# Performance work log

Measured on AMD Instinct MI355X. Metric: run time of the kernel, lower is better.

## Reference

```python
import jax, jax.numpy as jnp
import numpy as np

N_NODES = 100000
N_EDGES = 1600000
IN_FEAT = 512
HIDDEN = 128
N_CLASSES = 7


def gcn_conv(x, edge_index, edge_weight, W, b):
    """PyG GCNConv: add self-loops (weight 1), symmetric normalization, linear, scatter-add, bias."""
    n = x.shape[0]
    src = jnp.concatenate([edge_index[0], jnp.arange(n, dtype=edge_index.dtype)])
    dst = jnp.concatenate([edge_index[1], jnp.arange(n, dtype=edge_index.dtype)])
    w = jnp.concatenate([edge_weight, jnp.ones((n,), dtype=edge_weight.dtype)])
    deg = jax.ops.segment_sum(w, dst, num_segments=n)  # degree on destination (col)
    dinv = jnp.where(deg > 0, jax.lax.rsqrt(deg), 0.0)
    norm = dinv[src] * w * dinv[dst]                   # [E+N]
    h = x @ W                                          # [N, out] transform BEFORE propagate
    msg = h[src] * norm[:, None]                       # [E+N, out] irregular gather
    out = jax.ops.segment_sum(msg, dst, num_segments=n)  # scatter-reduce
    return out + b


def setup_inputs() -> dict:
    key = jax.random.key(0)
    k1, k2, k3, k4, k5, k6 = jax.random.split(key, 6)
    x = jax.random.normal(k1, (N_NODES, IN_FEAT), dtype=jnp.float32)
    edge_index = jax.random.randint(k2, (2, N_EDGES), 0, N_NODES, dtype=jnp.int32)
    edge_weight = jax.random.uniform(k3, (N_EDGES,), dtype=jnp.float32)
    s1 = 1.0 / np.sqrt(IN_FEAT)
    s2 = 1.0 / np.sqrt(HIDDEN)
    W1 = jax.random.uniform(k4, (IN_FEAT, HIDDEN), dtype=jnp.float32, minval=-s1, maxval=s1)
    b1 = jnp.zeros((HIDDEN,), dtype=jnp.float32)
    W2 = jax.random.uniform(k5, (HIDDEN, N_CLASSES), dtype=jnp.float32, minval=-s2, maxval=s2)
    b2 = jnp.zeros((N_CLASSES,), dtype=jnp.float32)
    return {"x": x, "edge_index": edge_index, "edge_weight": edge_weight,
            "W1": W1, "b1": b1, "W2": W2, "b2": b2}


def reference(x, edge_index, edge_weight, W1, b1, W2, b2):
    # eval mode: F.dropout(training=False) is identity
    h = jax.nn.elu(gcn_conv(x, edge_index, edge_weight, W1, b1))
    out = gcn_conv(h, edge_index, edge_weight, W2, b2)
    return jax.nn.log_softmax(out, axis=1)
```

## Files before the change

kernel.cpp:

```cpp
#include <hip/hip_runtime.h>
#include <hip/hip_bf16.h>
#include <math.h>

#define N_NODES 100000
#define N_EDGES 1600000
#define IN_F 512
#define HID 128
#define NCLS 7

#define DEG_SHIFT 43
#define DEG_WMASK ((1ull << 43) - 1)
#define DEG_SCALE 4194304.0f
#define DEG_INV_SCALE (1.0f / 4194304.0f)

typedef short short8 __attribute__((ext_vector_type(8)));
typedef float f32x4 __attribute__((ext_vector_type(4)));

__device__ __forceinline__ unsigned pack_bf16x2(float a, float b) {
  unsigned ua = __float_as_uint(a), ub = __float_as_uint(b);
  unsigned ra = (ua + 0x7FFFu + ((ua >> 16) & 1u)) >> 16;
  unsigned rb = (ub + 0x7FFFu + ((ub >> 16) & 1u)) >> 16;
  return ra | (rb << 16);
}
__device__ __forceinline__ unsigned short f32_to_bf16(float v) {
  unsigned u = __float_as_uint(v);
  return (unsigned short)((u + 0x7FFFu + ((u >> 16) & 1u)) >> 16);
}
__device__ __forceinline__ float bf_lo(unsigned u) { return __uint_as_float(u << 16); }
__device__ __forceinline__ float bf_hi(unsigned u) { return __uint_as_float(u & 0xFFFF0000u); }

__global__ void k_deg_count(const int* __restrict__ ei, const float* __restrict__ ew,
                            unsigned long long* __restrict__ packed, int* __restrict__ rank) {
  int e = blockIdx.x * blockDim.x + threadIdx.x;
  if (e >= N_EDGES) return;
  int d = ei[N_EDGES + e];
  unsigned long long fx = (unsigned long long)(ew[e] * DEG_SCALE + 0.5f);
  unsigned long long old = atomicAdd(&packed[d], (1ull << DEG_SHIFT) | fx);
  rank[e] = (int)(old >> DEG_SHIFT);
}

__global__ void k_dinv(const unsigned long long* __restrict__ packed,
                       float* __restrict__ dinv, int* __restrict__ cnt,
                       uint2* __restrict__ csr_pad) {
  int i = blockIdx.x * blockDim.x + threadIdx.x;
  if (i < 8) csr_pad[i] = make_uint2(0u, 0u);
  if (i >= N_NODES) return;
  unsigned long long p = packed[i];
  cnt[i] = (int)(p >> DEG_SHIFT);
  float wsum = (float)(p & DEG_WMASK) * DEG_INV_SCALE;
  dinv[i] = rsqrtf(wsum + 1.0f);
}

__global__ void k_w1t(const float* __restrict__ W1, unsigned* __restrict__ w1t_u) {
  int n = blockIdx.x;
  int t = threadIdx.x;
  float a = W1[(size_t)(2 * t) * HID + n];
  float b = W1[(size_t)(2 * t + 1) * HID + n];
  w1t_u[(size_t)n * 256 + t] = pack_bf16x2(a, b);
}

__global__ void k_scan_partial(const int* __restrict__ cnt, int* __restrict__ bsum) {
  __shared__ int s[256];
  int t = threadIdx.x;
  int base = blockIdx.x * 1024;
  int v = 0;
#pragma unroll
  for (int q = 0; q < 4; q++) {
    int idx = base + t * 4 + q;
    if (idx < N_NODES) v += cnt[idx];
  }
  s[t] = v;
  __syncthreads();
  for (int o = 128; o > 0; o >>= 1) {
    if (t < o) s[t] += s[t + o];
    __syncthreads();
  }
  if (t == 0) bsum[blockIdx.x] = s[0];
}

__global__ void k_scan_bsum(int* bsum, int nb) {
  if (threadIdx.x == 0 && blockIdx.x == 0) {
    int acc = 0;
    for (int i = 0; i < nb; i++) { int v = bsum[i]; bsum[i] = acc; acc += v; }
  }
}

__global__ void k_scan_final(const int* __restrict__ cnt, const int* __restrict__ bsum,
                             int* __restrict__ offs) {
  __shared__ int s[256];
  int t = threadIdx.x;
  int base = blockIdx.x * 1024;
  int v[4]; int sum = 0;
#pragma unroll
  for (int q = 0; q < 4; q++) {
    int idx = base + t * 4 + q;
    v[q] = (idx < N_NODES) ? cnt[idx] : 0;
    sum += v[q];
  }
  s[t] = sum;
  __syncthreads();
  for (int o = 1; o < 256; o <<= 1) {
    int x = (t >= o) ? s[t - o] : 0;
    __syncthreads();
    s[t] += x;
    __syncthreads();
  }
  int acc = s[t] - sum + bsum[blockIdx.x];
#pragma unroll
  for (int q = 0; q < 4; q++) {
    int idx = base + t * 4 + q;
    if (idx < N_NODES) offs[idx] = acc;
    acc += v[q];
  }
}

__global__ void k_fill(const int* __restrict__ ei, const float* __restrict__ ew,
                       const int* __restrict__ rank, const int* __restrict__ offs,
                       uint2* __restrict__ csr) {
  int e = blockIdx.x * blockDim.x + threadIdx.x;
  if (e >= N_EDGES) return;
  int sidx = ei[e];
  int d = ei[N_EDGES + e];
  int p = offs[d] + rank[e];
  csr[p] = make_uint2((unsigned)sidx, __float_as_uint(ew[e]));
}

#define G1_LDSROW 20
__global__ __launch_bounds__(256) void k_gemm1(const float* __restrict__ x,
                                               const unsigned* __restrict__ w1t_u,
                                               const float* __restrict__ dinv,
                                               unsigned short* __restrict__ h_u16) {
  __shared__ unsigned As[128 * G1_LDSROW];
  __shared__ unsigned Bs[128 * G1_LDSROW];
  const int tid = threadIdx.x;
  const int lane = tid & 63;
  const int w = tid >> 6;
  const int wr = w >> 1, wc = w & 1;
  const int quad = lane >> 4;
  const int l16 = lane & 15;
  const int m0 = blockIdx.x * 128;

  f32x4 acc[4][4];
#pragma unroll
  for (int i = 0; i < 4; i++)
#pragma unroll
    for (int j = 0; j < 4; j++) acc[i][j] = (f32x4){0.f, 0.f, 0.f, 0.f};

  for (int k0 = 0; k0 < IN_F; k0 += 32) {
    __syncthreads();
#pragma unroll
    for (int q = 0; q < 4; q++) {
      int flat = q * 256 + tid;
      int row = flat >> 3;
      int c4 = flat & 7;
      int gr = m0 + row;
      float4 v = make_float4(0.f, 0.f, 0.f, 0.f);
      if (gr < N_NODES) v = *(const float4*)(x + (size_t)gr * IN_F + k0 + c4 * 4);
      unsigned lo = pack_bf16x2(v.x, v.y);
      unsigned hi = pack_bf16x2(v.z, v.w);
      *(uint2*)&As[row * G1_LDSROW + c4 * 2] = make_uint2(lo, hi);
    }
#pragma unroll
    for (int q = 0; q < 2; q++) {
      int flat = q * 256 + tid;
      int row = flat >> 2;
      int c = flat & 3;
      uint4 bv = ((const uint4*)w1t_u)[(size_t)row * 64 + (k0 >> 3) + c];
      *(uint4*)&Bs[row * G1_LDSROW + c * 4] = bv;
    }
    __syncthreads();
    short8 af[4], bf[4];
#pragma unroll
    for (int mi = 0; mi < 4; mi++)
      af[mi] = *(const short8*)&As[(wr * 64 + mi * 16 + l16) * G1_LDSROW + quad * 4];
#pragma unroll
    for (int ni = 0; ni < 4; ni++)
      bf[ni] = *(const short8*)&Bs[(wc * 64 + ni * 16 + l16) * G1_LDSROW + quad * 4];
#pragma unroll
    for (int mi = 0; mi < 4; mi++)
#pragma unroll
      for (int ni = 0; ni < 4; ni++)
        acc[mi][ni] = __builtin_amdgcn_mfma_f32_16x16x32_bf16(af[mi], bf[ni], acc[mi][ni], 0, 0, 0);
  }
#pragma unroll
  for (int mi = 0; mi < 4; mi++) {
    float df[4];
#pragma unroll
    for (int r = 0; r < 4; r++) {
      int grow = m0 + wr * 64 + mi * 16 + quad * 4 + r;
      df[r] = (grow < N_NODES) ? dinv[grow] : 0.f;
    }
#pragma unroll
    for (int ni = 0; ni < 4; ni++) {
      int gcol = wc * 64 + ni * 16 + l16;
#pragma unroll
      for (int r = 0; r < 4; r++) {
        int grow = m0 + wr * 64 + mi * 16 + quad * 4 + r;
        if (grow < N_NODES)
          h_u16[(size_t)grow * HID + gcol] = f32_to_bf16(acc[mi][ni][r] * df[r]);
      }
    }
  }
}

__global__ __launch_bounds__(256) void k_agg1(const unsigned* __restrict__ h_u,
    const float* __restrict__ dinv, const int* __restrict__ offs, const int* __restrict__ cnt,
    const uint2* __restrict__ csr, const float* __restrict__ b1,
    unsigned* __restrict__ act1_u) {
  int i = blockIdx.x * 4 + (threadIdx.x >> 6);
  int lane = threadIdx.x & 63;
  if (i >= N_NODES) return;
  int start = offs[i], len = cnt[i];
  int end = start + len;
  float ax = 0.f, ay = 0.f;
  for (int p = start; p < end; p += 8) {
    uint2 e[8];
#pragma unroll
    for (int k = 0; k < 8; k++) e[k] = csr[p + k];
    unsigned u[8];
#pragma unroll
    for (int k = 0; k < 8; k++) u[k] = h_u[(size_t)e[k].x * 64 + lane];
#pragma unroll
    for (int k = 0; k < 8; k++) {
      float n = (k == 0 || p + k < end) ? __uint_as_float(e[k].y) : 0.f;
      ax = fmaf(bf_lo(u[k]), n, ax);
      ay = fmaf(bf_hi(u[k]), n, ay);
    }
  }
  float di = dinv[i];
  unsigned u = h_u[(size_t)i * 64 + lane];
  float2 bb = *(const float2*)(b1 + lane * 2);
  float vx = fmaf(di, ax + bf_lo(u), bb.x);
  float vy = fmaf(di, ay + bf_hi(u), bb.y);
  vx = vx > 0.f ? vx : expm1f(vx);
  vy = vy > 0.f ? vy : expm1f(vy);
  act1_u[(size_t)i * 64 + lane] = pack_bf16x2(vx, vy);
}

__global__ __launch_bounds__(256) void k_gemm2(const unsigned* __restrict__ act1_u,
                                               const float* __restrict__ W2,
                                               const float* __restrict__ dinv,
                                               float* __restrict__ h2) {
  __shared__ float sA[32][HID + 1];
  __shared__ float sW[HID * NCLS];
  const int tid = threadIdx.x;
  const int r0 = blockIdx.x * 32;
#pragma unroll
  for (int j = 0; j < 8; j++) {
    int idx = tid + j * 256;
    int row = idx >> 6;
    int c = idx & 63;
    unsigned u = act1_u[(size_t)(r0 + row) * 64 + c];
    sA[row][c * 2]     = bf_lo(u);
    sA[row][c * 2 + 1] = bf_hi(u);
  }
#pragma unroll
  for (int j = 0; j < 4; j++) {
    int idx = tid + j * 256;
    if (idx < HID * NCLS) sW[idx] = W2[idx];
  }
  __syncthreads();
  const int r = tid >> 3;
  const int c = tid & 7;
  float acc = 0.0f;
  if (c < NCLS) {
#pragma unroll 8
    for (int k = 0; k < HID; k++) acc = fmaf(sA[r][k], sW[k * NCLS + c], acc);
  }
  h2[(size_t)(r0 + r) * 8 + c] = acc * dinv[r0 + r];
}

__global__ __launch_bounds__(256) void k_agg2(const float* __restrict__ h2,
    const float* __restrict__ dinv, const int* __restrict__ offs, const int* __restrict__ cnt,
    const uint2* __restrict__ csr, const float* __restrict__ b2, float* __restrict__ out) {
  int tid = threadIdx.x;
  int i = blockIdx.x * 32 + (tid >> 3);
  int f = tid & 7;
  if (i >= N_NODES) return;
  int start = offs[i], len = cnt[i];
  int end = start + len;
  float acc = 0.0f;
  for (int p = start; p < end; p += 4) {
    uint2 e0 = csr[p];
    uint2 e1 = csr[p + 1];
    uint2 e2 = csr[p + 2];
    uint2 e3 = csr[p + 3];
    float v0 = h2[(size_t)e0.x * 8 + f];
    float v1 = h2[(size_t)e1.x * 8 + f];
    float v2 = h2[(size_t)e2.x * 8 + f];
    float v3 = h2[(size_t)e3.x * 8 + f];
    float n0 = __uint_as_float(e0.y);
    float n1 = (p + 1 < end) ? __uint_as_float(e1.y) : 0.f;
    float n2 = (p + 2 < end) ? __uint_as_float(e2.y) : 0.f;
    float n3 = (p + 3 < end) ? __uint_as_float(e3.y) : 0.f;
    acc = fmaf(v0, n0, acc);
    acc = fmaf(v1, n1, acc);
    acc = fmaf(v2, n2, acc);
    acc = fmaf(v3, n3, acc);
  }
  float di = dinv[i];
  float v = fmaf(di, acc + h2[(size_t)i * 8 + f], (f < NCLS) ? b2[f] : 0.0f);
  float vm = (f < NCLS) ? v : -INFINITY;
#pragma unroll
  for (int o = 1; o < 8; o <<= 1) vm = fmaxf(vm, __shfl_xor(vm, o, 8));
  float ex = (f < NCLS) ? expf(v - vm) : 0.0f;
  float s8 = ex;
#pragma unroll
  for (int o = 1; o < 8; o <<= 1) s8 += __shfl_xor(s8, o, 8);
  float lse = logf(s8);
  if (f < NCLS) out[(size_t)i * NCLS + f] = v - vm - lse;
}

extern "C" void kernel_launch(void* const* d_in, const int* in_sizes, int n_in,
                              void* d_out, int out_size, void* d_ws, size_t ws_size,
                              hipStream_t stream) {
  const float* x  = (const float*)d_in[0];
  const int*   ei = (const int*)d_in[1];
  const float* ew = (const float*)d_in[2];
  const float* W1 = (const float*)d_in[3];
  const float* b1 = (const float*)d_in[4];
  const float* W2 = (const float*)d_in[5];
  const float* b2 = (const float*)d_in[6];
  float* out = (float*)d_out;

  char* w = (char*)d_ws;
  const size_t Npad  = ((size_t)N_NODES * 4 + 255) & ~(size_t)255;
  const size_t Npad8 = ((size_t)N_NODES * 8 + 255) & ~(size_t)255;
  const size_t Epad  = ((size_t)N_EDGES * 4 + 255) & ~(size_t)255;
  size_t off = 0;
  unsigned long long* packed = (unsigned long long*)(w + off); off += Npad8;
  float*    dinv     = (float*)(w + off);    off += Npad;
  int*      cnt      = (int*)(w + off);      off += Npad;
  int*      offs     = (int*)(w + off);      off += Npad;
  int*      bsum     = (int*)(w + off);      off += 1024;
  int*      rank     = (int*)(w + off);      off += Epad;
  uint2*    csr      = (uint2*)(w + off);    off += ((size_t)(N_EDGES + 8) * 8 + 255) & ~(size_t)255;
  unsigned* w1t_u    = (unsigned*)(w + off); off += (size_t)HID * 256 * 4;
  unsigned short* h_u16 = (unsigned short*)(w + off); off += (size_t)N_NODES * HID * 2;
  unsigned* act1_u   = (unsigned*)(w + off); off += (size_t)N_NODES * 64 * 4;
  float*    h2       = (float*)(w + off);    off += (size_t)N_NODES * 8 * 4;

  hipMemsetAsync(packed, 0, Npad8, stream);

  k_deg_count<<<N_EDGES / 256, 256, 0, stream>>>(ei, ew, packed, rank);
  k_w1t<<<HID, 256, 0, stream>>>(W1, w1t_u);
  k_dinv<<<(N_NODES + 255) / 256, 256, 0, stream>>>(packed, dinv, cnt, csr + N_EDGES);
  const int nb = (N_NODES + 1023) / 1024;
  k_scan_partial<<<nb, 256, 0, stream>>>(cnt, bsum);
  k_scan_bsum<<<1, 64, 0, stream>>>(bsum, nb);
  k_scan_final<<<nb, 256, 0, stream>>>(cnt, bsum, offs);
  k_fill<<<N_EDGES / 256, 256, 0, stream>>>(ei, ew, rank, offs, csr);
  k_gemm1<<<(N_NODES + 127) / 128, 256, 0, stream>>>(x, w1t_u, dinv, h_u16);
  k_agg1<<<(N_NODES + 3) / 4, 256, 0, stream>>>((const unsigned*)h_u16, dinv, offs, cnt,
                                                csr, b1, act1_u);
  k_gemm2<<<N_NODES / 32, 256, 0, stream>>>(act1_u, W2, dinv, h2);
  k_agg2<<<N_NODES / 32, 256, 0, stream>>>(h2, dinv, offs, cnt, csr, b2, out);
}
```

Measured before the change: 594.3 us.

## Load GEMM1 MFMA fragments directly from global memory with register double-buffering

Drops the LDS staging and both __syncthreads from the x@W1 GEMM. Each lane now loads its MFMA A and B fragments straight from global memory, and the next k-step is prefetched into registers while the current step's MFMAs run. This removes LDS traffic and barrier stalls. In exchange, x is read redundantly by the two column-waves and loads become 32-byte per-row strided accesses that coalesce less well, and register pressure goes up.

```diff
diff --git a/kernel.cpp b/kernel.cpp
--- a/kernel.cpp
+++ b/kernel.cpp
@@ -125,13 +125,10 @@
   csr[p] = make_uint2((unsigned)sidx, __float_as_uint(ew[e]));
 }
 
-#define G1_LDSROW 20
 __global__ __launch_bounds__(256) void k_gemm1(const float* __restrict__ x,
                                                const unsigned* __restrict__ w1t_u,
                                                const float* __restrict__ dinv,
                                                unsigned short* __restrict__ h_u16) {
-  __shared__ unsigned As[128 * G1_LDSROW];
-  __shared__ unsigned Bs[128 * G1_LDSROW];
   const int tid = threadIdx.x;
   const int lane = tid & 63;
   const int w = tid >> 6;
@@ -140,47 +137,86 @@
   const int l16 = lane & 15;
   const int m0 = blockIdx.x * 128;
 
+  const float* arow[4];
+#pragma unroll
+  for (int mi = 0; mi < 4; mi++) {
+    int gr = m0 + wr * 64 + mi * 16 + l16;
+    if (gr > N_NODES - 1) gr = N_NODES - 1;
+    arow[mi] = x + (size_t)gr * IN_F + quad * 8;
+  }
+  const unsigned* brow[4];
+#pragma unroll
+  for (int ni = 0; ni < 4; ni++) {
+    int n = wc * 64 + ni * 16 + l16;
+    brow[ni] = w1t_u + (size_t)n * 256 + quad * 4;
+  }
+
   f32x4 acc[4][4];
 #pragma unroll
   for (int i = 0; i < 4; i++)
 #pragma unroll
     for (int j = 0; j < 4; j++) acc[i][j] = (f32x4){0.f, 0.f, 0.f, 0.f};
 
-  for (int k0 = 0; k0 < IN_F; k0 += 32) {
-    __syncthreads();
-#pragma unroll
-    for (int q = 0; q < 4; q++) {
-      int flat = q * 256 + tid;
-      int row = flat >> 3;
-      int c4 = flat & 7;
-      int gr = m0 + row;
-      float4 v = make_float4(0.f, 0.f, 0.f, 0.f);
-      if (gr < N_NODES) v = *(const float4*)(x + (size_t)gr * IN_F + k0 + c4 * 4);
-      unsigned lo = pack_bf16x2(v.x, v.y);
-      unsigned hi = pack_bf16x2(v.z, v.w);
-      *(uint2*)&As[row * G1_LDSROW + c4 * 2] = make_uint2(lo, hi);
-    }
-#pragma unroll
-    for (int q = 0; q < 2; q++) {
-      int flat = q * 256 + tid;
-      int row = flat >> 2;
-      int c = flat & 3;
-      uint4 bv = ((const uint4*)w1t_u)[(size_t)row * 64 + (k0 >> 3) + c];
-      *(uint4*)&Bs[row * G1_LDSROW + c * 4] = bv;
-    }
-    __syncthreads();
-    short8 af[4], bf[4];
+  float4 a_cur[4][2];
+  uint4 b_cur[4];
+#pragma unroll
+  for (int mi = 0; mi < 4; mi++) {
+    a_cur[mi][0] = *(const float4*)(arow[mi]);
+    a_cur[mi][1] = *(const float4*)(arow[mi] + 4);
+  }
+#pragma unroll
+  for (int ni = 0; ni < 4; ni++) b_cur[ni] = *(const uint4*)(brow[ni]);
+
+  for (int step = 0; step < 15; step++) {
+    float4 a_nxt[4][2];
+    uint4 b_nxt[4];
+    const int ko = (step + 1) * 32;
+    const int kd = (step + 1) * 16;
+#pragma unroll
+    for (int mi = 0; mi < 4; mi++) {
+      a_nxt[mi][0] = *(const float4*)(arow[mi] + ko);
+      a_nxt[mi][1] = *(const float4*)(arow[mi] + ko + 4);
+    }
+#pragma unroll
+    for (int ni = 0; ni < 4; ni++) b_nxt[ni] = *(const uint4*)(brow[ni] + kd);
+    short8 af[4];
+#pragma unroll
+    for (int mi = 0; mi < 4; mi++) {
+      union { short8 s; unsigned u[4]; } t;
+      t.u[0] = pack_bf16x2(a_cur[mi][0].x, a_cur[mi][0].y);
+      t.u[1] = pack_bf16x2(a_cur[mi][0].z, a_cur[mi][0].w);
+      t.u[2] = pack_bf16x2(a_cur[mi][1].x, a_cur[mi][1].y);
+      t.u[3] = pack_bf16x2(a_cur[mi][1].z, a_cur[mi][1].w);
+      af[mi] = t.s;
+    }
 #pragma unroll
     for (int mi = 0; mi < 4; mi++)
-      af[mi] = *(const short8*)&As[(wr * 64 + mi * 16 + l16) * G1_LDSROW + quad * 4];
-#pragma unroll
-    for (int ni = 0; ni < 4; ni++)
-      bf[ni] = *(const short8*)&Bs[(wc * 64 + ni * 16 + l16) * G1_LDSROW + quad * 4];
+#pragma unroll
+      for (int ni = 0; ni < 4; ni++)
+        acc[mi][ni] = __builtin_amdgcn_mfma_f32_16x16x32_bf16(
+            af[mi], *(const short8*)&b_cur[ni], acc[mi][ni], 0, 0, 0);
+#pragma unroll
+    for (int mi = 0; mi < 4; mi++) { a_cur[mi][0] = a_nxt[mi][0]; a_cur[mi][1] = a_nxt[mi][1]; }
+#pragma unroll
+    for (int ni = 0; ni < 4; ni++) b_cur[ni] = b_nxt[ni];
+  }
+  {
+    short8 af[4];
+#pragma unroll
+    for (int mi = 0; mi < 4; mi++) {
+      union { short8 s; unsigned u[4]; } t;
+      t.u[0] = pack_bf16x2(a_cur[mi][0].x, a_cur[mi][0].y);
+      t.u[1] = pack_bf16x2(a_cur[mi][0].z, a_cur[mi][0].w);
+      t.u[2] = pack_bf16x2(a_cur[mi][1].x, a_cur[mi][1].y);
+      t.u[3] = pack_bf16x2(a_cur[mi][1].z, a_cur[mi][1].w);
+      af[mi] = t.s;
+    }
 #pragma unroll
     for (int mi = 0; mi < 4; mi++)
 #pragma unroll
       for (int ni = 0; ni < 4; ni++)
-        acc[mi][ni] = __builtin_amdgcn_mfma_f32_16x16x32_bf16(af[mi], bf[ni], acc[mi][ni], 0, 0, 0);
+        acc[mi][ni] = __builtin_amdgcn_mfma_f32_16x16x32_bf16(
+            af[mi], *(const short8*)&b_cur[ni], acc[mi][ni], 0, 0, 0);
   }
 #pragma unroll
   for (int mi = 0; mi < 4; mi++) {
```

Result: faster. 570.0 us (-4.1%).

## Restructure GEMM1 into per-wave 16-row tiles with pre-swizzled bf16 W1 fragments

Applied to the files above, without the earlier changes.

Each wave now computes its own 16-row by 128-column output tile. It stages only its own x rows into a private LDS slab and uses __threadfence_block instead of block-wide barriers. W1 is pre-packed into MFMA fragment order, so B operands are loaded straight from global memory (likely L2/cache resident) with no LDS staging. The goal is to remove block-level syncs and raise the number of small independent blocks, so the x streaming, which is the dominant memory traffic, flows with more parallelism. The cost is that every wave re-reads the full W1 from cache, and A-operand LDS reuse across waves is lost.

```diff
diff --git a/kernel.cpp b/kernel.cpp
--- a/kernel.cpp
+++ b/kernel.cpp
@@ -51,12 +51,19 @@
   dinv[i] = rsqrtf(wsum + 1.0f);
 }
 
-__global__ void k_w1t(const float* __restrict__ W1, unsigned* __restrict__ w1t_u) {
-  int n = blockIdx.x;
-  int t = threadIdx.x;
-  float a = W1[(size_t)(2 * t) * HID + n];
-  float b = W1[(size_t)(2 * t + 1) * HID + n];
-  w1t_u[(size_t)n * 256 + t] = pack_bf16x2(a, b);
+__global__ void k_w1t(const float* __restrict__ W1, uint4* __restrict__ w1bf) {
+  int idx = blockIdx.x * 256 + threadIdx.x;
+  int lane = idx & 63;
+  int st = idx >> 6;
+  int t = st & 7, s = st >> 3;
+  int n = t * 16 + (lane & 15);
+  int k0 = s * 32 + (lane >> 4) * 8;
+  uint4 v;
+  v.x = pack_bf16x2(W1[(size_t)(k0 + 0) * HID + n], W1[(size_t)(k0 + 1) * HID + n]);
+  v.y = pack_bf16x2(W1[(size_t)(k0 + 2) * HID + n], W1[(size_t)(k0 + 3) * HID + n]);
+  v.z = pack_bf16x2(W1[(size_t)(k0 + 4) * HID + n], W1[(size_t)(k0 + 5) * HID + n]);
+  v.w = pack_bf16x2(W1[(size_t)(k0 + 6) * HID + n], W1[(size_t)(k0 + 7) * HID + n]);
+  w1bf[idx] = v;
 }
 
 __global__ void k_scan_partial(const int* __restrict__ cnt, int* __restrict__ bsum) {
@@ -125,82 +132,64 @@
   csr[p] = make_uint2((unsigned)sidx, __float_as_uint(ew[e]));
 }
 
-#define G1_LDSROW 20
+#define SLABSTRIDE 132
 __global__ __launch_bounds__(256) void k_gemm1(const float* __restrict__ x,
-                                               const unsigned* __restrict__ w1t_u,
+                                               const uint4* __restrict__ w1bf,
                                                const float* __restrict__ dinv,
                                                unsigned short* __restrict__ h_u16) {
-  __shared__ unsigned As[128 * G1_LDSROW];
-  __shared__ unsigned Bs[128 * G1_LDSROW];
+  __shared__ unsigned slab[4 * 16 * SLABSTRIDE];
   const int tid = threadIdx.x;
   const int lane = tid & 63;
-  const int w = tid >> 6;
-  const int wr = w >> 1, wc = w & 1;
-  const int quad = lane >> 4;
-  const int l16 = lane & 15;
-  const int m0 = blockIdx.x * 128;
-
-  f32x4 acc[4][4];
-#pragma unroll
-  for (int i = 0; i < 4; i++)
-#pragma unroll
-    for (int j = 0; j < 4; j++) acc[i][j] = (f32x4){0.f, 0.f, 0.f, 0.f};
-
-  for (int k0 = 0; k0 < IN_F; k0 += 32) {
-    __syncthreads();
-#pragma unroll
-    for (int q = 0; q < 4; q++) {
-      int flat = q * 256 + tid;
-      int row = flat >> 3;
-      int c4 = flat & 7;
-      int gr = m0 + row;
-      float4 v = make_float4(0.f, 0.f, 0.f, 0.f);
-      if (gr < N_NODES) v = *(const float4*)(x + (size_t)gr * IN_F + k0 + c4 * 4);
-      unsigned lo = pack_bf16x2(v.x, v.y);
-      unsigned hi = pack_bf16x2(v.z, v.w);
-      *(uint2*)&As[row * G1_LDSROW + c4 * 2] = make_uint2(lo, hi);
-    }
-#pragma unroll
-    for (int q = 0; q < 2; q++) {
-      int flat = q * 256 + tid;
-      int row = flat >> 2;
-      int c = flat & 3;
-      uint4 bv = ((const uint4*)w1t_u)[(size_t)row * 64 + (k0 >> 3) + c];
-      *(uint4*)&Bs[row * G1_LDSROW + c * 4] = bv;
-    }
-    __syncthreads();
-    short8 af[4], bf[4];
-#pragma unroll
-    for (int mi = 0; mi < 4; mi++)
-      af[mi] = *(const short8*)&As[(wr * 64 + mi * 16 + l16) * G1_LDSROW + quad * 4];
-#pragma unroll
-    for (int ni = 0; ni < 4; ni++)
-      bf[ni] = *(const short8*)&Bs[(wc * 64 + ni * 16 + l16) * G1_LDSROW + quad * 4];
-#pragma unroll
-    for (int mi = 0; mi < 4; mi++)
-#pragma unroll
-      for (int ni = 0; ni < 4; ni++)
-        acc[mi][ni] = __builtin_amdgcn_mfma_f32_16x16x32_bf16(af[mi], bf[ni], acc[mi][ni], 0, 0, 0);
-  }
-#pragma unroll
-  for (int mi = 0; mi < 4; mi++) {
-    float df[4];
-#pragma unroll
-    for (int r = 0; r < 4; r++) {
-      int grow = m0 + wr * 64 + mi * 16 + quad * 4 + r;
-      df[r] = (grow < N_NODES) ? dinv[grow] : 0.f;
-    }
-#pragma unroll
-    for (int ni = 0; ni < 4; ni++) {
-      int gcol = wc * 64 + ni * 16 + l16;
-#pragma unroll
-      for (int r = 0; r < 4; r++) {
-        int grow = m0 + wr * 64 + mi * 16 + quad * 4 + r;
-        if (grow < N_NODES)
-          h_u16[(size_t)grow * HID + gcol] = f32_to_bf16(acc[mi][ni][r] * df[r]);
+  const int wv = tid >> 6;
+  const int gw = blockIdx.x * 4 + wv;
+  if (gw >= N_NODES / 16) return;
+  const int m0 = gw * 16;
+  unsigned* ws = slab + wv * 16 * SLABSTRIDE;
+  const int l16 = lane & 15, quad = lane >> 4;
+
+  f32x4 acc[8];
+#pragma unroll
+  for (int t = 0; t < 8; t++) acc[t] = (f32x4){0.f, 0.f, 0.f, 0.f};
+
+#pragma unroll
+  for (int hf = 0; hf < 2; hf++) {
+#pragma unroll
+    for (int b = 0; b < 2; b++) {
+      float4 v[8];
+#pragma unroll
+      for (int i = 0; i < 8; i++) {
+        int row = b * 8 + i;
+        v[i] = *(const float4*)(x + (size_t)(m0 + row) * IN_F + hf * 256 + lane * 4);
+      }
+#pragma unroll
+      for (int i = 0; i < 8; i++) {
+        int row = b * 8 + i;
+        unsigned lo = pack_bf16x2(v[i].x, v[i].y);
+        unsigned hi = pack_bf16x2(v[i].z, v[i].w);
+        *(uint2*)&ws[row * SLABSTRIDE + lane * 2] = make_uint2(lo, hi);
       }
     }
-  }
+    __threadfence_block();
+#pragma unroll
+    for (int ks = 0; ks < 8; ks++) {
+      short8 af = *(const short8*)&ws[l16 * SLABSTRIDE + ks * 16 + quad * 4];
+      const uint4* bbase = w1bf + (size_t)(hf * 8 + ks) * 8 * 64 + lane;
+#pragma unroll
+      for (int t = 0; t < 8; t++) {
+        uint4 bv = bbase[t * 64];
+        acc[t] = __builtin_amdgcn_mfma_f32_16x16x32_bf16(af, *(const short8*)&bv,
+                                                         acc[t], 0, 0, 0);
+      }
+    }
+  }
+  float df[4];
+#pragma unroll
+  for (int r = 0; r < 4; r++) df[r] = dinv[m0 + quad * 4 + r];
+#pragma unroll
+  for (int t = 0; t < 8; t++)
+#pragma unroll
+    for (int r = 0; r < 4; r++)
+      h_u16[(size_t)(m0 + quad * 4 + r) * HID + t * 16 + l16] = f32_to_bf16(acc[t][r] * df[r]);
 }
 
 __global__ __launch_bounds__(256) void k_agg1(const unsigned* __restrict__ h_u,
@@ -335,7 +324,7 @@
   int*      bsum     = (int*)(w + off);      off += 1024;
   int*      rank     = (int*)(w + off);      off += Epad;
   uint2*    csr      = (uint2*)(w + off);    off += ((size_t)(N_EDGES + 8) * 8 + 255) & ~(size_t)255;
-  unsigned* w1t_u    = (unsigned*)(w + off); off += (size_t)HID * 256 * 4;
+  uint4*    w1bf     = (uint4*)(w + off);    off += (size_t)8192 * 16;
   unsigned short* h_u16 = (unsigned short*)(w + off); off += (size_t)N_NODES * HID * 2;
   unsigned* act1_u   = (unsigned*)(w + off); off += (size_t)N_NODES * 64 * 4;
   float*    h2       = (float*)(w + off);    off += (size_t)N_NODES * 8 * 4;
@@ -343,14 +332,15 @@
   hipMemsetAsync(packed, 0, Npad8, stream);
 
   k_deg_count<<<N_EDGES / 256, 256, 0, stream>>>(ei, ew, packed, rank);
-  k_w1t<<<HID, 256, 0, stream>>>(W1, w1t_u);
+  k_w1t<<<32, 256, 0, stream>>>(W1, w1bf);
   k_dinv<<<(N_NODES + 255) / 256, 256, 0, stream>>>(packed, dinv, cnt, csr + N_EDGES);
   const int nb = (N_NODES + 1023) / 1024;
   k_scan_partial<<<nb, 256, 0, stream>>>(cnt, bsum);
   k_scan_bsum<<<1, 64, 0, stream>>>(bsum, nb);
   k_scan_final<<<nb, 256, 0, stream>>>(cnt, bsum, offs);
   k_fill<<<N_EDGES / 256, 256, 0, stream>>>(ei, ew, rank, offs, csr);
-  k_gemm1<<<(N_NODES + 127) / 128, 256, 0, stream>>>(x, w1t_u, dinv, h_u16);
+  const int g1_waves = N_NODES / 16;
+  k_gemm1<<<(g1_waves + 3) / 4, 256, 0, stream>>>(x, w1bf, dinv, h_u16);
   k_agg1<<<(N_NODES + 3) / 4, 256, 0, stream>>>((const unsigned*)h_u16, dinv, offs, cnt,
                                                 csr, b1, act1_u);
   k_gemm2<<<N_NODES / 32, 256, 0, stream>>>(act1_u, W2, dinv, h2);
```

After: 549.2 us. 7.6% less time.
